# Kernel optimization log

Hardware: AMD Instinct MI355X
Metric: run time of the kernel (lower is better)

Reference implementation:

```python
import jax, jax.numpy as jnp
import numpy as np


def setup_inputs() -> dict:
    key = jax.random.key(0)
    k1, k2, k3 = jax.random.split(key, 3)
    B, D, L = 32768, 1024, 2
    return {
        "x": jax.random.normal(k1, (B, D), dtype=jnp.float32),
        "local_angles": jax.random.normal(k2, (L, D), dtype=jnp.float32),
        "ent_angles": jax.random.normal(k3, (L, D // 2), dtype=jnp.float32),
    }


def _local_layer(out, angles):
    # Sequential chain of Givens rotations on column pairs (i, (i+1)%D).
    # Each step uses the already-updated columns, exactly like the torch loop
    # (out = out @ R.T  ==  rotate columns i and j of out).
    D = out.shape[1]
    idx = jnp.arange(D)

    def body(o, inp):
        i, theta = inp
        j = (i + 1) % D
        c, s = jnp.cos(theta), jnp.sin(theta)
        ci = jnp.take(o, i, axis=1)  # [B]
        cj = jnp.take(o, j, axis=1)  # [B]
        o = o.at[:, i].set(c * ci - s * cj)
        o = o.at[:, j].set(s * ci + c * cj)
        return o, None

    out, _ = jax.lax.scan(body, out, (idx, angles))
    return out


def _ent_layer(out, angles):
    # Entangler rotations act on disjoint pairs (2k, 2k+1) -> fully vectorized.
    B, D = out.shape
    p = out.reshape(B, D // 2, 2)
    c, s = jnp.cos(angles), jnp.sin(angles)  # [D//2]
    x0, x1 = p[..., 0], p[..., 1]
    return jnp.stack([c * x0 - s * x1, s * x0 + c * x1], axis=-1).reshape(B, D)


def reference(x, local_angles, ent_angles):
    out = x
    num_layers = local_angles.shape[0]
    for l in range(num_layers):
        out = _local_layer(out, local_angles[l])
        out = _ent_layer(out, ent_angles[l])
    return out
```

## Files before the change

### kernel.cpp

```cpp
#include <hip/hip_runtime.h>

#define D_DIM    1024
#define PER_LANE 16
#define NLAYER   2
#define NPAIR    8
#define WPB      4

__device__ __forceinline__ int swz(int c) { return c ^ ((c >> 3) & 7); }

__global__ __launch_bounds__(256) void qent_kernel(
        const float* __restrict__ x,
        const float* __restrict__ local_angles,
        const float* __restrict__ ent_angles,
        float* __restrict__ out, int B)
{
    const int lane  = threadIdx.x & 63;
    const int wid   = threadIdx.x >> 6;
    const int gwave = blockIdx.x * WPB + wid;
    const int nwave = gridDim.x * WPB;

    __shared__ float lds_cl[NLAYER][PER_LANE][64];
    __shared__ float lds_sl[NLAYER][PER_LANE][64];
    __shared__ float lds_ce[NLAYER][NPAIR][64];
    __shared__ float lds_se[NLAYER][NPAIR][64];
    __shared__ float4 tb[WPB][256];

    for (int idx = threadIdx.x; idx < NLAYER * D_DIM; idx += blockDim.x) {
        int L = idx >> 10, i = idx & (D_DIM - 1);
        int ln = i >> 4, k = i & 15;
        float s, c;
        sincosf(local_angles[idx], &s, &c);
        lds_cl[L][k][ln] = c;
        lds_sl[L][k][ln] = s;
    }
    for (int idx = threadIdx.x; idx < NLAYER * (D_DIM / 2); idx += blockDim.x) {
        int L = idx >> 9, p = idx & (D_DIM / 2 - 1);
        int ln = p >> 3, m = p & 7;
        float s, c;
        sincosf(ent_angles[idx], &s, &c);
        lds_ce[L][m][ln] = c;
        lds_se[L][m][ln] = s;
    }
    __syncthreads();

    float cl[NLAYER][PER_LANE], sl[NLAYER][PER_LANE];
    float ce[NLAYER][NPAIR],    se[NLAYER][NPAIR];
    #pragma unroll
    for (int L = 0; L < NLAYER; ++L) {
        #pragma unroll
        for (int k = 0; k < PER_LANE; ++k) {
            cl[L][k] = lds_cl[L][k][lane];
            sl[L][k] = lds_sl[L][k][lane];
        }
        #pragma unroll
        for (int m = 0; m < NPAIR; ++m) {
            ce[L][m] = lds_ce[L][m][lane];
            se[L][m] = lds_se[L][m][lane];
        }
    }

    for (int row = gwave; row < B; row += nwave) {
        const float4* rp =
            reinterpret_cast<const float4*>(x + (size_t)row * D_DIM);
        float4 ld[4];
        #pragma unroll
        for (int q = 0; q < 4; ++q) ld[q] = rp[q * 64 + lane];
        #pragma unroll
        for (int q = 0; q < 4; ++q) tb[wid][swz(q * 64 + lane)] = ld[q];

        float v[PER_LANE];
        #pragma unroll
        for (int r = 0; r < 4; ++r) {
            float4 t = tb[wid][swz(4 * lane + r)];
            v[4*r+0] = t.x; v[4*r+1] = t.y; v[4*r+2] = t.z; v[4*r+3] = t.w;
        }

        #pragma unroll
        for (int L = 0; L < NLAYER; ++L) {
            float vnf = __shfl_down(v[0], 1);

            float A = 1.f, Bv = 0.f;
            #pragma unroll
            for (int k = 0; k < PER_LANE; ++k) {
                float vn = (k < PER_LANE - 1) ? v[k + 1] : vnf;
                Bv = sl[L][k] * Bv + cl[L][k] * vn;
                A  = sl[L][k] * A;
            }

            float Ai = A, Bi = Bv;
            #pragma unroll
            for (int dd = 1; dd < 64; dd <<= 1) {
                float Au = __shfl_up(Ai, dd);
                float Bu = __shfl_up(Bi, dd);
                if (lane >= dd) {
                    Bi = Ai * Bu + Bi;
                    Ai = Ai * Au;
                }
            }
            float Ax  = __shfl_up(Ai, 1);
            float Bx  = __shfl_up(Bi, 1);
            float v0b = __shfl(v[0], 0);
            float u   = (lane == 0) ? v[0] : (Ax * v0b + Bx);

            #pragma unroll
            for (int k = 0; k < PER_LANE - 1; ++k) {
                float vn = v[k + 1];
                float f  = cl[L][k] * u - sl[L][k] * vn;
                u        = sl[L][k] * u + cl[L][k] * vn;
                v[k] = f;
            }
            float a0   = __shfl(v[0], 0);
            float vn15 = (lane == 63) ? a0 : vnf;
            float f15  = cl[L][PER_LANE-1] * u - sl[L][PER_LANE-1] * vn15;
            float un   = sl[L][PER_LANE-1] * u + cl[L][PER_LANE-1] * vn15;
            v[PER_LANE-1] = f15;
            float f0new = __shfl(un, 63);
            if (lane == 0) v[0] = f0new;

            #pragma unroll
            for (int m = 0; m < NPAIR; ++m) {
                float x0 = v[2*m], x1 = v[2*m+1];
                v[2*m]   = ce[L][m] * x0 - se[L][m] * x1;
                v[2*m+1] = se[L][m] * x0 + ce[L][m] * x1;
            }
        }

        #pragma unroll
        for (int r = 0; r < 4; ++r) {
            float4 t;
            t.x = v[4*r+0]; t.y = v[4*r+1]; t.z = v[4*r+2]; t.w = v[4*r+3];
            tb[wid][swz(4 * lane + r)] = t;
        }
        float4* op = reinterpret_cast<float4*>(out + (size_t)row * D_DIM);
        float4 st[4];
        #pragma unroll
        for (int q = 0; q < 4; ++q) st[q] = tb[wid][swz(q * 64 + lane)];
        #pragma unroll
        for (int q = 0; q < 4; ++q) op[q * 64 + lane] = st[q];
    }
}

extern "C" void kernel_launch(void* const* d_in, const int* in_sizes, int n_in,
                              void* d_out, int out_size, void* d_ws, size_t ws_size,
                              hipStream_t stream) {
    const float* x  = (const float*)d_in[0];
    const float* la = (const float*)d_in[1];
    const float* ea = (const float*)d_in[2];
    float* out = (float*)d_out;
    int B = in_sizes[0] / D_DIM;
    qent_kernel<<<2048, 256, 0, stream>>>(x, la, ea, out, B);
}
```

Measured before the change: 67.13 us.

## Precompute rotation tables in separate kernel and double-buffer rows via async LDS loads

Moves the sincos of all angles into a small pre-kernel that writes a cos/sin table to workspace. The main kernel reads the local cos/sin directly from global memory with float4 loads, and reads the entangler coefficients from LDS inside the loop instead of holding them in registers. Each wave now handles a fixed 8 rows, and each row is brought from global straight into double-buffered LDS with global_load_lds, so the next row's load can overlap the current row's compute. The costs are an extra kernel launch, a grid size that assumes B is divisible by 32, and a full vmcnt(0) wait that also waits on the previous row's stores.

```diff
diff --git a/kernel.cpp b/kernel.cpp
--- a/kernel.cpp
+++ b/kernel.cpp
@@ -5,73 +5,88 @@
 #define NLAYER   2
 #define NPAIR    8
 #define WPB      4
+#define ROWS_PW  8
 
 __device__ __forceinline__ int swz(int c) { return c ^ ((c >> 3) & 7); }
 
-__global__ __launch_bounds__(256) void qent_kernel(
+__global__ void angles_kernel(const float* __restrict__ la,
+                              const float* __restrict__ ea,
+                              float* __restrict__ tab) {
+    int t  = blockIdx.x * blockDim.x + threadIdx.x;
+    int nt = gridDim.x * blockDim.x;
+    for (int i = t; i < NLAYER * D_DIM; i += nt) {
+        float s, c; sincosf(la[i], &s, &c);
+        tab[i] = c; tab[2048 + i] = s;
+    }
+    for (int i = t; i < NLAYER * (D_DIM / 2); i += nt) {
+        float s, c; sincosf(ea[i], &s, &c);
+        tab[4096 + i] = c; tab[5120 + i] = s;
+    }
+}
+
+__global__ __launch_bounds__(256, 4) void qent_kernel(
         const float* __restrict__ x,
-        const float* __restrict__ local_angles,
-        const float* __restrict__ ent_angles,
+        const float* __restrict__ tab,
         float* __restrict__ out, int B)
 {
-    const int lane  = threadIdx.x & 63;
-    const int wid   = threadIdx.x >> 6;
+    const int lane = threadIdx.x & 63;
+    const int wid  = threadIdx.x >> 6;
     const int gwave = blockIdx.x * WPB + wid;
-    const int nwave = gridDim.x * WPB;
 
-    __shared__ float lds_cl[NLAYER][PER_LANE][64];
-    __shared__ float lds_sl[NLAYER][PER_LANE][64];
-    __shared__ float lds_ce[NLAYER][NPAIR][64];
-    __shared__ float lds_se[NLAYER][NPAIR][64];
-    __shared__ float4 tb[WPB][256];
+    __shared__ float4 buf[WPB][2][256];
+    __shared__ float  lds_ce[NLAYER][NPAIR][64];
+    __shared__ float  lds_se[NLAYER][NPAIR][64];
 
-    for (int idx = threadIdx.x; idx < NLAYER * D_DIM; idx += blockDim.x) {
-        int L = idx >> 10, i = idx & (D_DIM - 1);
-        int ln = i >> 4, k = i & 15;
-        float s, c;
-        sincosf(local_angles[idx], &s, &c);
-        lds_cl[L][k][ln] = c;
-        lds_sl[L][k][ln] = s;
-    }
-    for (int idx = threadIdx.x; idx < NLAYER * (D_DIM / 2); idx += blockDim.x) {
-        int L = idx >> 9, p = idx & (D_DIM / 2 - 1);
-        int ln = p >> 3, m = p & 7;
-        float s, c;
-        sincosf(ent_angles[idx], &s, &c);
-        lds_ce[L][m][ln] = c;
-        lds_se[L][m][ln] = s;
+    for (int t = threadIdx.x; t < NLAYER * 512; t += 256) {
+        int L = t >> 9, p = t & 511;
+        int m = p >> 6, ln = p & 63;
+        lds_ce[L][m][ln] = tab[4096 + L * 512 + ln * 8 + m];
+        lds_se[L][m][ln] = tab[5120 + L * 512 + ln * 8 + m];
     }
     __syncthreads();
 
     float cl[NLAYER][PER_LANE], sl[NLAYER][PER_LANE];
-    float ce[NLAYER][NPAIR],    se[NLAYER][NPAIR];
     #pragma unroll
     for (int L = 0; L < NLAYER; ++L) {
+        const float4* cp = reinterpret_cast<const float4*>(tab + L * D_DIM + lane * PER_LANE);
+        const float4* sp = reinterpret_cast<const float4*>(tab + 2048 + L * D_DIM + lane * PER_LANE);
         #pragma unroll
-        for (int k = 0; k < PER_LANE; ++k) {
-            cl[L][k] = lds_cl[L][k][lane];
-            sl[L][k] = lds_sl[L][k][lane];
-        }
-        #pragma unroll
-        for (int m = 0; m < NPAIR; ++m) {
-            ce[L][m] = lds_ce[L][m][lane];
-            se[L][m] = lds_se[L][m][lane];
+        for (int q = 0; q < 4; ++q) {
+            float4 c4 = cp[q], s4 = sp[q];
+            cl[L][4*q+0] = c4.x; cl[L][4*q+1] = c4.y; cl[L][4*q+2] = c4.z; cl[L][4*q+3] = c4.w;
+            sl[L][4*q+0] = s4.x; sl[L][4*q+1] = s4.y; sl[L][4*q+2] = s4.z; sl[L][4*q+3] = s4.w;
         }
     }
 
-    for (int row = gwave; row < B; row += nwave) {
-        const float4* rp =
-            reinterpret_cast<const float4*>(x + (size_t)row * D_DIM);
-        float4 ld[4];
+    const int l2 = lane ^ (lane >> 3);
+    auto stage = [&](int b, int row) {
+        const float* src = x + (size_t)row * D_DIM;
         #pragma unroll
-        for (int q = 0; q < 4; ++q) ld[q] = rp[q * 64 + lane];
-        #pragma unroll
-        for (int q = 0; q < 4; ++q) tb[wid][swz(q * 64 + lane)] = ld[q];
+        for (int q = 0; q < 4; ++q) {
+            const float* gp = src + q * 256 + l2 * 4;
+            void* lp = (void*)&buf[wid][b][q * 64];
+            __builtin_amdgcn_global_load_lds(
+                (const __attribute__((address_space(1))) void*)gp,
+                (__attribute__((address_space(3))) void*)lp, 16, 0, 0);
+        }
+    };
+
+    const int row0 = gwave * ROWS_PW;
+    stage(0, row0);
+
+    #pragma unroll
+    for (int it = 0; it < ROWS_PW; ++it) {
+        const int cur = it & 1;
+        const int row = row0 + it;
+
+        asm volatile("s_waitcnt vmcnt(0)" ::: "memory");
+
+        if (it + 1 < ROWS_PW) stage(cur ^ 1, row + 1);
 
         float v[PER_LANE];
         #pragma unroll
         for (int r = 0; r < 4; ++r) {
-            float4 t = tb[wid][swz(4 * lane + r)];
+            float4 t = buf[wid][cur][swz(4 * lane + r)];
             v[4*r+0] = t.x; v[4*r+1] = t.y; v[4*r+2] = t.z; v[4*r+3] = t.w;
         }
 
@@ -119,9 +134,11 @@
 
             #pragma unroll
             for (int m = 0; m < NPAIR; ++m) {
+                float cem = lds_ce[L][m][lane];
+                float sem = lds_se[L][m][lane];
                 float x0 = v[2*m], x1 = v[2*m+1];
-                v[2*m]   = ce[L][m] * x0 - se[L][m] * x1;
-                v[2*m+1] = se[L][m] * x0 + ce[L][m] * x1;
+                v[2*m]   = cem * x0 - sem * x1;
+                v[2*m+1] = sem * x0 + cem * x1;
             }
         }
 
@@ -129,14 +146,14 @@
         for (int r = 0; r < 4; ++r) {
             float4 t;
             t.x = v[4*r+0]; t.y = v[4*r+1]; t.z = v[4*r+2]; t.w = v[4*r+3];
-            tb[wid][swz(4 * lane + r)] = t;
+            buf[wid][cur][swz(4 * lane + r)] = t;
         }
         float4* op = reinterpret_cast<float4*>(out + (size_t)row * D_DIM);
-        float4 st[4];
         #pragma unroll
-        for (int q = 0; q < 4; ++q) st[q] = tb[wid][swz(q * 64 + lane)];
-        #pragma unroll
-        for (int q = 0; q < 4; ++q) op[q * 64 + lane] = st[q];
+        for (int q = 0; q < 4; ++q) {
+            float4 t = buf[wid][cur][swz(q * 64 + lane)];
+            op[q * 64 + lane] = t;
+        }
     }
 }
 
@@ -147,6 +164,10 @@
     const float* la = (const float*)d_in[1];
     const float* ea = (const float*)d_in[2];
     float* out = (float*)d_out;
+    float* tab = (float*)d_ws;
     int B = in_sizes[0] / D_DIM;
-    qent_kernel<<<2048, 256, 0, stream>>>(x, la, ea, out, B);
+
+    angles_kernel<<<8, 256, 0, stream>>>(la, ea, tab);
+    int blocks = B / (WPB * ROWS_PW);
+    qent_kernel<<<blocks, 256, 0, stream>>>(x, tab, out, B);
 }
```

Result: slower. 204.4 us (+204.5%).
